# Kernel tuning notes

Measured on AMD Instinct MI355X. Metric: run time of the kernel, lower is better.

The kernel has to match this reference:

```python
import jax, jax.numpy as jnp
from jax import lax
import numpy as np

K = 3  # kernel size per dim, dimension=6 -> 3**6 = 729 taps
OFFS = np.stack(np.meshgrid(*([np.arange(K)] * 6), indexing='ij'), axis=-1).reshape(-1, 6).astype(np.int32)


def conv6d(x, kernel):
    """Dense emulation of a 1->1 channel MinkowskiConvolution over 6 spatial dims.

    x: (b, s, s, d, d, d, d) with zeros at absent sparse coordinates.
    kernel: (729,) flattened 3^6 kernel (in=out=1 channel, no bias).
    Zeros at absent coordinates contribute nothing to the gathered sums, so the
    dense conv equals the sparse conv evaluated everywhere.
    """
    xp = jnp.pad(x, [(0, 0)] + [(1, 1)] * 6)
    offs = jnp.asarray(OFFS)
    zero = jnp.int32(0)

    def body(acc, ow):
        off, wt = ow
        sl = lax.dynamic_slice(
            xp, (zero, off[0], off[1], off[2], off[3], off[4], off[5]), x.shape)
        return acc + wt * sl, None

    acc, _ = lax.scan(jax.checkpoint(body), jnp.zeros_like(x), (offs, kernel))
    return acc


def _transpose6d(t):
    # swap the two scale dims and the two image-coordinate pairs:
    # (b, s1, s2, h1, w1, h2, w2) -> (b, s2, s1, h2, w2, h1, w1)
    return jnp.transpose(t, (0, 2, 1, 5, 6, 3, 4))


def setup_inputs() -> dict:
    key = jax.random.key(0)
    k1, k2 = jax.random.split(key)
    x = jax.random.normal(k1, (1, 2, 2, 32, 32, 32, 32), dtype=jnp.float32)
    kernel = jax.random.normal(k2, (K ** 6,), dtype=jnp.float32) * 0.05
    return {"x": x, "kernel": kernel}


def reference(x, kernel):
    # MinkowskiConvolution outputs at the input coordinate set; MinkowskiSigmoid
    # acts on features at those coordinates; to_dense() zero-fills elsewhere.
    # Dense equivalent: mask to the input nonzero set.
    mask = (x != 0).astype(x.dtype)
    branch = lambda z: jax.nn.sigmoid(conv6d(jax.nn.relu(z), kernel))
    # symmetric mode: conv(x) + T(conv(T(x))); T(coords(T(x))) == coords(x)
    y = mask * (branch(x) + _transpose6d(branch(_transpose6d(x))))
    b, s1, s2, d1, d2, d3, d4 = y.shape
    y = y.reshape(b, s1 * s2, d1, d2, d3, d4).sum(axis=1)  # (b, h1, w1, h2, w2)
    return y
```

## Files before the change

### kernel.cpp

```cpp
#include <hip/hip_runtime.h>

typedef _Float16 half8 __attribute__((ext_vector_type(8)));
typedef float f16v __attribute__((ext_vector_type(16)));
typedef float f4 __attribute__((ext_vector_type(4)));
typedef unsigned long long ull;

#define X_SLAB   1048576
#define PLANE_BYTES (34*36*4*2)
#define RPT_SITES (34*34*34*36)
#define RPT_OFF  65536
#define RPT_SLACK 4096
#define TAB_N    (3*6*3*512)
#define TAB_ELEMS  (4*81*8)

__global__ __launch_bounds__(256)
void prep(const float* __restrict__ x, const float* __restrict__ w,
          ull* __restrict__ rpt, _Float16* __restrict__ tabm) {
    unsigned s = blockIdx.x * 256 + threadIdx.x;
    if (s < RPT_SITES) {
        unsigned q = s;
        int j4 = q % 36; q /= 36;
        int j3 = q % 34; q /= 34;
        int j2 = q % 34; q /= 34;
        int j1 = q;
        union { _Float16 h[4]; ull u; } pk;
        pk.u = 0ull;
        if (j1 >= 1 && j1 <= 32 && j2 >= 1 && j2 <= 32 &&
            j3 >= 1 && j3 <= 32 && j4 >= 1 && j4 <= 32) {
            size_t off = (size_t)(j1-1)*32768 + (j2-1)*1024 + (j3-1)*32 + (j4-1);
            #pragma unroll
            for (int t = 0; t < 4; ++t)
                pk.h[t] = (_Float16)fmaxf(x[(size_t)t*X_SLAB + off], 0.f);
        }
        rpt[s] = pk.u;
    }
    if (blockIdx.x == 0) {
        for (int idx = threadIdx.x; idx < TAB_N; idx += 256) {
            int j = idx & 7, l = (idx >> 3) & 63, slice = idx >> 9;
            int p4 = slice % 3, j2rel = (slice/3) % 6, p2 = slice/18;
            int n32 = l & 31;
            int d2 = n32 >> 3, n8 = n32 & 7;
            int k = 8*(l>>5) + j;
            int p5h = k >> 2, t = k & 3;
            int p3 = j2rel - d2;
            float val = 0.f;
            if (p5h < 3 && p3 >= 0 && p3 <= 2) {
                int br = n8 & 1, sc = n8 >> 1, s1 = sc >> 1, s2 = sc & 1;
                int t1 = t >> 1, t2 = t & 1;
                int a = t1 - s1 + 1, b = t2 - s2 + 1;
                int widx = (br == 0)
                    ? (a*243 + b*81 + p2*27 + p3*9 + p4*3 + p5h)
                    : (b*243 + a*81 + p4*27 + p5h*9 + p2*3 + p3);
                val = w[widx];
            }
            tabm[idx] = (_Float16)val;
        }
    }
}

__global__ __launch_bounds__(256)
void conv_mfma(const float* __restrict__ x, const ull* __restrict__ rpt,
               const _Float16* __restrict__ tabm, float* __restrict__ out) {
    __shared__ __align__(16) unsigned char stg[4][2][2048];
    __shared__ unsigned char msk[2048];

    const int tid  = threadIdx.x;
    const int lane = tid & 63;
    const int wv   = tid >> 6;
    const int e2b  = blockIdx.x * 4;
    const int e1   = blockIdx.y;
    const int bz   = blockIdx.z;
    const size_t pbase = (size_t)e1*32768 + (size_t)e2b*1024 + (size_t)bz*512;

    {
        int p0 = tid * 8;
        int d2 = p0 >> 9, rem = p0 & 511;
        const float* xb = x + pbase + (size_t)d2*1024 + rem;
        #pragma unroll
        for (int g = 0; g < 2; ++g) {
            f4 a0 = *(const f4*)(xb + (size_t)0*X_SLAB + 4*g);
            f4 a1 = *(const f4*)(xb + (size_t)1*X_SLAB + 4*g);
            f4 a2 = *(const f4*)(xb + (size_t)2*X_SLAB + 4*g);
            f4 a3 = *(const f4*)(xb + (size_t)3*X_SLAB + 4*g);
            unsigned wbits = 0;
            #pragma unroll
            for (int q = 0; q < 4; ++q) {
                unsigned b = (a0[q] != 0.f ? 1u : 0u) | (a1[q] != 0.f ? 2u : 0u)
                           | (a2[q] != 0.f ? 4u : 0u) | (a3[q] != 0.f ? 8u : 0u);
                wbits |= b << (8*q);
            }
            *(unsigned*)&msk[p0 + 4*g] = wbits;
        }
    }
    __syncthreads();

    f16v acc[4];
    #pragma unroll
    for (int r = 0; r < 4; ++r)
        #pragma unroll
        for (int i = 0; i < 16; ++i) acc[r][i] = 0.f;

    const int R     = bz*16 + wv*4;
    const int j4off = (lane & 31)*8 + (lane >> 5)*16;
    const char* aglob0 = (const char*)rpt + (size_t)R*288 + lane*16;

    auto stage_to = [&](int it, int slot) {
        int p2 = it / 6, j2 = it - p2*6;
        const char* src = aglob0 + ((size_t)(e1+p2)*34 + (e2b+j2))*PLANE_BYTES;
        unsigned char* dst = &stg[wv][slot][0] + lane*16;
        #pragma unroll
        for (int k = 0; k < 2; ++k)
            __builtin_amdgcn_global_load_lds(
                (const __attribute__((address_space(1))) unsigned int*)(src + k*1024),
                (__attribute__((address_space(3))) unsigned int*)(dst + k*1024),
                16, 0, 0);
    };
    auto loadB = [&](int it, half8* B) {
        const _Float16* tb = tabm + it*1536 + lane*8;
        B[0] = *(const half8*)(tb);
        B[1] = *(const half8*)(tb + 512);
        B[2] = *(const half8*)(tb + 1024);
    };
    auto compute = [&](int slot, const half8* B) {
        const unsigned char* sb = &stg[wv][slot][0];
        union { ull u[2]; half8 h; } A[6];
        #pragma unroll
        for (int j3l = 0; j3l < 6; ++j3l) {
            const ull* ap = (const ull*)(sb + j3l*288 + j4off);
            A[j3l].u[0] = ap[0];
            A[j3l].u[1] = ap[1];
        }
        #pragma unroll
        for (int j3l = 0; j3l < 6; ++j3l) {
            if (j3l <= 3)
                acc[j3l]   = __builtin_amdgcn_mfma_f32_32x32x16_f16(A[j3l].h, B[0], acc[j3l],   0,0,0);
            if (j3l >= 1 && j3l <= 4)
                acc[j3l-1] = __builtin_amdgcn_mfma_f32_32x32x16_f16(A[j3l].h, B[1], acc[j3l-1], 0,0,0);
            if (j3l >= 2)
                acc[j3l-2] = __builtin_amdgcn_mfma_f32_32x32x16_f16(A[j3l].h, B[2], acc[j3l-2], 0,0,0);
        }
    };

    half8 Ba[3], Bb[3];
    stage_to(0, 0);
    loadB(0, Ba);

    #pragma unroll 1
    for (int ip = 0; ip < 9; ++ip) {
        const int itE = 2*ip;
        {
            int nit = itE + 1;
            stage_to(nit, 1);
            loadB(nit, Bb);
            asm volatile("s_waitcnt vmcnt(5)" ::: "memory");
            compute(0, Ba);
        }
        {
            int nit = (itE + 2 < 18) ? itE + 2 : 17;
            stage_to(nit, 0);
            loadB(nit, Ba);
            asm volatile("s_waitcnt vmcnt(5)" ::: "memory");
            compute(1, Bb);
        }
    }

    const int n8 = lane & 7;
    const int d2 = (lane >> 3) & 3;
    const int h  = lane >> 5;
    const int sbit = n8 >> 1;
    float* outp = out + pbase + (size_t)d2*1024;
    #pragma unroll
    for (int rloc = 0; rloc < 4; ++rloc) {
        const int e3loc = wv*4 + rloc;
        float v[16];
        #pragma unroll
        for (int g = 0; g < 4; ++g) {
            unsigned mw = *(const unsigned*)&msk[d2*512 + e3loc*32 + 8*g + 4*h];
            #pragma unroll
            for (int j = 0; j < 4; ++j) {
                float a  = acc[rloc][4*g + j];
                float sg = __builtin_amdgcn_rcpf(1.f + __expf(-a));
                v[4*g+j] = ((mw >> (8*j + sbit)) & 1u) ? sg : 0.f;
            }
        }
        #pragma unroll
        for (int i = 0; i < 16; ++i) {
            v[i] += __shfl_xor(v[i], 1);
            v[i] += __shfl_xor(v[i], 2);
            v[i] += __shfl_xor(v[i], 4);
        }
        if (n8 == 0) {
            #pragma unroll
            for (int g = 0; g < 4; ++g) {
                f4 o; o.x = v[4*g]; o.y = v[4*g+1]; o.z = v[4*g+2]; o.w = v[4*g+3];
                *(f4*)(outp + e3loc*32 + 8*g + 4*h) = o;
            }
        }
    }
}

__global__ void build_wtab(const float* __restrict__ w, float* __restrict__ tab) {
    int idx = blockIdx.x * blockDim.x + threadIdx.x;
    if (idx >= TAB_ELEMS) return;
    int n  = idx & 7;
    int r  = idx >> 3;
    int p5 = r % 3; r /= 3;
    int p4 = r % 3; r /= 3;
    int p3 = r % 3; r /= 3;
    int p2 = r % 3; r /= 3;
    int t  = r;
    int t1 = t >> 1, t2 = t & 1;
    int br = n & 1;
    int s  = n >> 1;
    int s1 = s >> 1, s2 = s & 1;
    int a = t1 - s1 + 1;
    int b = t2 - s2 + 1;
    int widx = (br == 0)
        ? (a*243 + b*81 + p2*27 + p3*9 + p4*3 + p5)
        : (b*243 + a*81 + p4*27 + p5*9 + p2*3 + p3);
    tab[idx] = w[widx];
}

__global__ __launch_bounds__(256)
void conv_fp32(const float* __restrict__ x,
               const float* __restrict__ tab,
               float* __restrict__ out) {
    const int e4 = threadIdx.x;
    const int e3 = blockIdx.x * 8 + threadIdx.y;
    const int e2 = blockIdx.y;
    const int e1 = blockIdx.z;

    float acc[8];
    #pragma unroll
    for (int n = 0; n < 8; ++n) acc[n] = 0.f;

    #pragma unroll 1
    for (int t = 0; t < 4; ++t) {
        const float* st  = x + (size_t)t * X_SLAB;
        const float* wt0 = tab + t * 648;
        #pragma unroll
        for (int p2 = 0; p2 < 3; ++p2) {
            #pragma unroll
            for (int p3 = 0; p3 < 3; ++p3) {
                int i1 = e1 + p2 - 1, i2 = e2 + p3 - 1;
                bool v12 = ((unsigned)i1 < 32u) && ((unsigned)i2 < 32u);
                const float* base = st + (i1*32768 + i2*1024 + (e3-1)*32 + (e4-1));
                const float* wt = wt0 + (p2*3 + p3) * 72;
                #pragma unroll
                for (int p4 = 0; p4 < 3; ++p4) {
                    int i3 = e3 + p4 - 1;
                    bool v3 = v12 && ((unsigned)i3 < 32u);
                    #pragma unroll
                    for (int p5 = 0; p5 < 3; ++p5) {
                        int i4 = e4 + p5 - 1;
                        bool ok = v3 && ((unsigned)i4 < 32u);
                        float v = ok ? fmaxf(base[p4*32 + p5], 0.f) : 0.f;
                        const float* w8 = wt + (p4*3 + p5)*8;
                        #pragma unroll
                        for (int n = 0; n < 8; ++n)
                            acc[n] = fmaf(w8[n], v, acc[n]);
                    }
                }
            }
        }
    }

    const size_t eflat = (size_t)e1*32768 + e2*1024 + e3*32 + e4;
    float res = 0.f;
    #pragma unroll
    for (int i = 0; i < 4; ++i) {
        float xv = x[(size_t)i * X_SLAB + eflat];
        float s0 = __builtin_amdgcn_rcpf(1.f + __expf(-acc[2*i]));
        float s1 = __builtin_amdgcn_rcpf(1.f + __expf(-acc[2*i+1]));
        float m  = (xv != 0.f) ? 1.f : 0.f;
        res = fmaf(m, s0 + s1, res);
    }
    out[eflat] = res;
}

extern "C" void kernel_launch(void* const* d_in, const int* in_sizes, int n_in,
                              void* d_out, int out_size, void* d_ws, size_t ws_size,
                              hipStream_t stream) {
    const float* x = (const float*)d_in[0];
    const float* w = (const float*)d_in[1];
    float* out = (float*)d_out;

    const size_t need = (size_t)RPT_OFF + (size_t)RPT_SITES*8ull + RPT_SLACK;

    if (ws_size >= need) {
        _Float16* tabm = (_Float16*)d_ws;
        ull*      rpt  = (ull*)((char*)d_ws + RPT_OFF);
        prep<<<dim3((RPT_SITES + 255)/256), dim3(256), 0, stream>>>(x, w, rpt, tabm);
        dim3 grd(8, 32, 2), blk(256, 1, 1);
        conv_mfma<<<grd, blk, 0, stream>>>(x, rpt, tabm, out);
    } else {
        float* tab = (float*)d_ws;
        build_wtab<<<dim3((TAB_ELEMS + 255)/256), dim3(256), 0, stream>>>(w, tab);
        dim3 blk(32, 8, 1), grd(4, 32, 32);
        conv_fp32<<<grd, blk, 0, stream>>>(x, tab, out);
    }
}
```

Measured before the change: 97.69 us.

## Precompute nonzero mask in prep and split conv into twice as many blocks

Measured after the change: 98.14 us. Within noise of the previous version (+0.5%).

```diff
diff --git a/kernel.cpp b/kernel.cpp
--- a/kernel.cpp
+++ b/kernel.cpp
@@ -10,12 +10,14 @@
 #define RPT_SITES (34*34*34*36)
 #define RPT_OFF  65536
 #define RPT_SLACK 4096
+#define MSK_OFF  (RPT_OFF + RPT_SITES*8 + RPT_SLACK)
 #define TAB_N    (3*6*3*512)
 #define TAB_ELEMS  (4*81*8)
 
 __global__ __launch_bounds__(256)
 void prep(const float* __restrict__ x, const float* __restrict__ w,
-          ull* __restrict__ rpt, _Float16* __restrict__ tabm) {
+          ull* __restrict__ rpt, unsigned char* __restrict__ mskb,
+          _Float16* __restrict__ tabm) {
     unsigned s = blockIdx.x * 256 + threadIdx.x;
     if (s < RPT_SITES) {
         unsigned q = s;
@@ -28,9 +30,14 @@
         if (j1 >= 1 && j1 <= 32 && j2 >= 1 && j2 <= 32 &&
             j3 >= 1 && j3 <= 32 && j4 >= 1 && j4 <= 32) {
             size_t off = (size_t)(j1-1)*32768 + (j2-1)*1024 + (j3-1)*32 + (j4-1);
-            #pragma unroll
-            for (int t = 0; t < 4; ++t)
-                pk.h[t] = (_Float16)fmaxf(x[(size_t)t*X_SLAB + off], 0.f);
+            unsigned nib = 0;
+            #pragma unroll
+            for (int t = 0; t < 4; ++t) {
+                float v = x[(size_t)t*X_SLAB + off];
+                nib |= (v != 0.f ? 1u : 0u) << t;
+                pk.h[t] = (_Float16)fmaxf(v, 0.f);
+            }
+            mskb[off] = (unsigned char)nib;
         }
         rpt[s] = pk.u;
     }
@@ -59,10 +66,9 @@
 }
 
 __global__ __launch_bounds__(256)
-void conv_mfma(const float* __restrict__ x, const ull* __restrict__ rpt,
+void conv_mfma(const ull* __restrict__ rpt, const unsigned char* __restrict__ mskb,
                const _Float16* __restrict__ tabm, float* __restrict__ out) {
     __shared__ __align__(16) unsigned char stg[4][2][2048];
-    __shared__ unsigned char msk[2048];
 
     const int tid  = threadIdx.x;
     const int lane = tid & 63;
@@ -70,37 +76,14 @@
     const int e2b  = blockIdx.x * 4;
     const int e1   = blockIdx.y;
     const int bz   = blockIdx.z;
-    const size_t pbase = (size_t)e1*32768 + (size_t)e2b*1024 + (size_t)bz*512;
-
-    {
-        int p0 = tid * 8;
-        int d2 = p0 >> 9, rem = p0 & 511;
-        const float* xb = x + pbase + (size_t)d2*1024 + rem;
-        #pragma unroll
-        for (int g = 0; g < 2; ++g) {
-            f4 a0 = *(const f4*)(xb + (size_t)0*X_SLAB + 4*g);
-            f4 a1 = *(const f4*)(xb + (size_t)1*X_SLAB + 4*g);
-            f4 a2 = *(const f4*)(xb + (size_t)2*X_SLAB + 4*g);
-            f4 a3 = *(const f4*)(xb + (size_t)3*X_SLAB + 4*g);
-            unsigned wbits = 0;
-            #pragma unroll
-            for (int q = 0; q < 4; ++q) {
-                unsigned b = (a0[q] != 0.f ? 1u : 0u) | (a1[q] != 0.f ? 2u : 0u)
-                           | (a2[q] != 0.f ? 4u : 0u) | (a3[q] != 0.f ? 8u : 0u);
-                wbits |= b << (8*q);
-            }
-            *(unsigned*)&msk[p0 + 4*g] = wbits;
-        }
-    }
-    __syncthreads();
-
-    f16v acc[4];
-    #pragma unroll
-    for (int r = 0; r < 4; ++r)
+
+    f16v acc[2];
+    #pragma unroll
+    for (int r = 0; r < 2; ++r)
         #pragma unroll
         for (int i = 0; i < 16; ++i) acc[r][i] = 0.f;
 
-    const int R     = bz*16 + wv*4;
+    const int R     = bz*8 + wv*2;
     const int j4off = (lane & 31)*8 + (lane >> 5)*16;
     const char* aglob0 = (const char*)rpt + (size_t)R*288 + lane*16;
 
@@ -123,21 +106,17 @@
     };
     auto compute = [&](int slot, const half8* B) {
         const unsigned char* sb = &stg[wv][slot][0];
-        union { ull u[2]; half8 h; } A[6];
-        #pragma unroll
-        for (int j3l = 0; j3l < 6; ++j3l) {
+        union { ull u[2]; half8 h; } A[4];
+        #pragma unroll
+        for (int j3l = 0; j3l < 4; ++j3l) {
             const ull* ap = (const ull*)(sb + j3l*288 + j4off);
             A[j3l].u[0] = ap[0];
             A[j3l].u[1] = ap[1];
         }
         #pragma unroll
-        for (int j3l = 0; j3l < 6; ++j3l) {
-            if (j3l <= 3)
-                acc[j3l]   = __builtin_amdgcn_mfma_f32_32x32x16_f16(A[j3l].h, B[0], acc[j3l],   0,0,0);
-            if (j3l >= 1 && j3l <= 4)
-                acc[j3l-1] = __builtin_amdgcn_mfma_f32_32x32x16_f16(A[j3l].h, B[1], acc[j3l-1], 0,0,0);
-            if (j3l >= 2)
-                acc[j3l-2] = __builtin_amdgcn_mfma_f32_32x32x16_f16(A[j3l].h, B[2], acc[j3l-2], 0,0,0);
+        for (int p4 = 0; p4 < 3; ++p4) {
+            acc[0] = __builtin_amdgcn_mfma_f32_32x32x16_f16(A[p4  ].h, B[p4], acc[0], 0,0,0);
+            acc[1] = __builtin_amdgcn_mfma_f32_32x32x16_f16(A[p4+1].h, B[p4], acc[1], 0,0,0);
         }
     };
 
@@ -149,9 +128,8 @@
     for (int ip = 0; ip < 9; ++ip) {
         const int itE = 2*ip;
         {
-            int nit = itE + 1;
-            stage_to(nit, 1);
-            loadB(nit, Bb);
+            stage_to(itE + 1, 1);
+            loadB(itE + 1, Bb);
             asm volatile("s_waitcnt vmcnt(5)" ::: "memory");
             compute(0, Ba);
         }
@@ -168,14 +146,14 @@
     const int d2 = (lane >> 3) & 3;
     const int h  = lane >> 5;
     const int sbit = n8 >> 1;
-    float* outp = out + pbase + (size_t)d2*1024;
-    #pragma unroll
-    for (int rloc = 0; rloc < 4; ++rloc) {
-        const int e3loc = wv*4 + rloc;
+    const size_t colbase = (size_t)e1*32768 + (size_t)(e2b + d2)*1024;
+    #pragma unroll
+    for (int rloc = 0; rloc < 2; ++rloc) {
+        const int e3 = R + rloc;
         float v[16];
         #pragma unroll
         for (int g = 0; g < 4; ++g) {
-            unsigned mw = *(const unsigned*)&msk[d2*512 + e3loc*32 + 8*g + 4*h];
+            unsigned mw = *(const unsigned*)&mskb[colbase + e3*32 + 8*g + 4*h];
             #pragma unroll
             for (int j = 0; j < 4; ++j) {
                 float a  = acc[rloc][4*g + j];
@@ -193,7 +171,7 @@
             #pragma unroll
             for (int g = 0; g < 4; ++g) {
                 f4 o; o.x = v[4*g]; o.y = v[4*g+1]; o.z = v[4*g+2]; o.w = v[4*g+3];
-                *(f4*)(outp + e3loc*32 + 8*g + 4*h) = o;
+                *(f4*)(out + colbase + e3*32 + 8*g + 4*h) = o;
             }
         }
     }
@@ -285,14 +263,15 @@
     const float* w = (const float*)d_in[1];
     float* out = (float*)d_out;
 
-    const size_t need = (size_t)RPT_OFF + (size_t)RPT_SITES*8ull + RPT_SLACK;
+    const size_t need = (size_t)MSK_OFF + (size_t)X_SLAB;
 
     if (ws_size >= need) {
-        _Float16* tabm = (_Float16*)d_ws;
-        ull*      rpt  = (ull*)((char*)d_ws + RPT_OFF);
-        prep<<<dim3((RPT_SITES + 255)/256), dim3(256), 0, stream>>>(x, w, rpt, tabm);
-        dim3 grd(8, 32, 2), blk(256, 1, 1);
-        conv_mfma<<<grd, blk, 0, stream>>>(x, rpt, tabm, out);
+        _Float16*      tabm = (_Float16*)d_ws;
+        ull*           rpt  = (ull*)((char*)d_ws + RPT_OFF);
+        unsigned char* mskb = (unsigned char*)d_ws + MSK_OFF;
+        prep<<<dim3((RPT_SITES + 255)/256), dim3(256), 0, stream>>>(x, w, rpt, mskb, tabm);
+        dim3 grd(8, 32, 4), blk(256, 1, 1);
+        conv_mfma<<<grd, blk, 0, stream>>>(rpt, mskb, tabm, out);
     } else {
         float* tab = (float*)d_ws;
         build_wtab<<<dim3((TAB_ELEMS + 255)/256), dim3(256), 0, stream>>>(w, tab);
```
